# Kernel tuning notes

Measured on AMD Instinct MI355X. Metric: run time of the kernel, lower is better.

## Reference

```python
import jax, jax.numpy as jnp
import numpy as np

D_MODEL = 1024
N_HEADS = 16
D_K = D_MODEL // N_HEADS


def setup_inputs() -> dict:
    key = jax.random.key(0)
    k1, k2, k3, k4, k5 = jax.random.split(key, 5)
    B, S = 2, 2048
    scale = 1.0 / np.sqrt(D_MODEL)
    return {
        "query": jax.random.normal(k1, (B, S, D_MODEL), dtype=jnp.float32),
        "mask": jnp.ones((B, S, S), dtype=jnp.int32),
        "W_qkv": jax.random.normal(k2, (D_MODEL, 3 * D_MODEL), dtype=jnp.float32) * scale,
        "b_qkv": jax.random.normal(k3, (3 * D_MODEL,), dtype=jnp.float32) * 0.02,
        "W_out": jax.random.normal(k4, (D_MODEL, D_MODEL), dtype=jnp.float32) * scale,
        "b_out": jax.random.normal(k5, (D_MODEL,), dtype=jnp.float32) * 0.02,
    }


def reference(query, mask, W_qkv, b_qkv, W_out, b_out):
    B, S, _ = query.shape
    # fused QKV projection (all from query, matching the torch module)
    qkv = query @ W_qkv + b_qkv                      # [B, S, 3*D]
    q, k, v = jnp.split(qkv, 3, axis=-1)
    # [B, H, S, d_k]
    q = q.reshape(B, S, N_HEADS, D_K).transpose(0, 2, 1, 3)
    k = k.reshape(B, S, N_HEADS, D_K).transpose(0, 2, 1, 3)
    v = v.reshape(B, S, N_HEADS, D_K).transpose(0, 2, 1, 3)
    # scaled dot-product attention with explicit scores
    scores = jnp.einsum("bhqd,bhkd->bhqk", q, k) / jnp.sqrt(jnp.float32(D_K))
    m = mask[:, None, :, :]                           # [B, 1, S, S] broadcast over heads
    scores = jnp.where(m == 0, jnp.float32(-1e9), scores)
    attn = jax.nn.softmax(scores, axis=-1)           # dropout p=0 in eval -> identity
    ctx = jnp.einsum("bhqk,bhkd->bhqd", attn, v)     # [B, H, S, d_k]
    ctx = ctx.transpose(0, 2, 1, 3).reshape(B, S, D_MODEL)
    return ctx @ W_out + b_out
```

## Files before the change

kernel.cpp:

```cpp
#include <hip/hip_runtime.h>
#include <stdint.h>
#include <stddef.h>

#define S_LEN 2048
#define NB    2
#define DM    1024
#define NH    16
#define DKH   64
#define NTOK  4096
#define QKV_N 3072
#define QSCALE 0.18033688f

typedef __attribute__((ext_vector_type(4))) float floatx4;
using half2v = __attribute__((ext_vector_type(2))) _Float16;
using half4v = __attribute__((ext_vector_type(4))) _Float16;
using half8v = __attribute__((ext_vector_type(8))) _Float16;
using fp16x2 = __attribute__((ext_vector_type(2))) __fp16;

#if __has_builtin(__builtin_amdgcn_exp2f)
#define EXP2F __builtin_amdgcn_exp2f
#else
#define EXP2F exp2f
#endif

__device__ __forceinline__ void glds16(const void* g, void* l) {
    __builtin_amdgcn_global_load_lds((const __attribute__((address_space(1))) void*)g,
                                     (__attribute__((address_space(3))) void*)l,
                                     16, 0, 0);
}

__global__ __launch_bounds__(256) void cast_f16_kernel(const float* __restrict__ in,
                                                       _Float16* __restrict__ out, int n4) {
    int i = blockIdx.x * blockDim.x + threadIdx.x;
    if (i < n4) {
        float4 v = ((const float4*)in)[i];
        half4v o = {(_Float16)v.x, (_Float16)v.y, (_Float16)v.z, (_Float16)v.w};
        ((half4v*)out)[i] = o;
    }
}

__global__ __launch_bounds__(1024) void transpose_cast_kernel(const float* __restrict__ in,
                                                              _Float16* __restrict__ out,
                                                              int R, int C) {
    __shared__ float t[32][33];
    int c0 = blockIdx.x * 32, r0 = blockIdx.y * 32;
    int x = threadIdx.x, y = threadIdx.y;
    t[y][x] = in[(size_t)(r0 + y) * C + c0 + x];
    __syncthreads();
    out[(size_t)(c0 + y) * R + r0 + x] = (_Float16)t[x][y];
}

__global__ void flag_init_kernel(int* f) { *f = 1; }

__global__ __launch_bounds__(256) void mask_reduce_kernel(const int* __restrict__ mask,
                                                          int* __restrict__ f, int n4) {
    int i = blockIdx.x * blockDim.x + threadIdx.x;
    if (i < n4) {
        int4 v = ((const int4*)mask)[i];
        if (v.x == 0 || v.y == 0 || v.z == 0 || v.w == 0) *f = 0;
    }
}

template <int FINAL, int BN>
__global__ __launch_bounds__(256) void gemm_bt_kernel(const _Float16* __restrict__ A,
                                                      const _Float16* __restrict__ Bt,
                                                      const float* __restrict__ bias,
                                                      float* __restrict__ Cf,
                                                      _Float16* __restrict__ Ch,
                                                      _Float16* __restrict__ Vt,
                                                      int M, int N, int K) {
    constexpr int NJ = BN / 32;
    __shared__ _Float16 As[128 * 64];
    __shared__ _Float16 Bs[BN * 64];

    const int nt = blockIdx.x, mt = blockIdx.y;
    const int tid = threadIdx.x, wave = tid >> 6, lane = tid & 63;
    const int quad = lane >> 4, l16 = lane & 15;
    const int wm = wave >> 1, wn = wave & 1;

    floatx4 acc[4][NJ];
    #pragma unroll
    for (int i = 0; i < 4; ++i)
        #pragma unroll
        for (int j = 0; j < NJ; ++j)
            #pragma unroll
            for (int r = 0; r < 4; ++r) acc[i][j][r] = 0.0f;

    const _Float16* Ab = A + (size_t)mt * 128 * K;
    const _Float16* Bb = Bt + (size_t)nt * BN * K;

    for (int kt = 0; kt < K; kt += 64) {
        #pragma unroll
        for (int p = 0; p < 4; ++p) {
            int slot = p * 256 + wave * 64 + lane;
            int row = slot >> 3, cc = slot & 7, c = cc ^ (row & 7);
            glds16(Ab + (size_t)row * K + kt + c * 8, As + (size_t)(p * 256 + wave * 64) * 8);
        }
        #pragma unroll
        for (int p = 0; p < BN / 32; ++p) {
            int slot = p * 256 + wave * 64 + lane;
            int row = slot >> 3, cc = slot & 7, c = cc ^ (row & 7);
            glds16(Bb + (size_t)row * K + kt + c * 8, Bs + (size_t)(p * 256 + wave * 64) * 8);
        }
        __syncthreads();

        #pragma unroll
        for (int kk = 0; kk < 2; ++kk) {
            half8v af[4], bfr[NJ];
            #pragma unroll
            for (int i = 0; i < 4; ++i) {
                int row = wm * 64 + i * 16 + l16;
                int c = (kk * 4 + quad) ^ (row & 7);
                af[i] = *(const half8v*)(As + row * 64 + c * 8);
            }
            #pragma unroll
            for (int j = 0; j < NJ; ++j) {
                int row = wn * (BN / 2) + j * 16 + l16;
                int c = (kk * 4 + quad) ^ (row & 7);
                bfr[j] = *(const half8v*)(Bs + row * 64 + c * 8);
            }
            #pragma unroll
            for (int i = 0; i < 4; ++i)
                #pragma unroll
                for (int j = 0; j < NJ; ++j)
                    acc[i][j] = __builtin_amdgcn_mfma_f32_16x16x32_f16(af[i], bfr[j], acc[i][j], 0, 0, 0);
        }
        __syncthreads();
    }

    #pragma unroll
    for (int j = 0; j < NJ; ++j) {
        int n = nt * BN + wn * (BN / 2) + j * 16 + l16;
        float bv = bias[n];
        #pragma unroll
        for (int i = 0; i < 4; ++i) {
            int m0 = mt * 128 + wm * 64 + i * 16 + quad * 4;
            float v[4];
            #pragma unroll
            for (int r = 0; r < 4; ++r) v[r] = acc[i][j][r] + bv;
            if (FINAL) {
                #pragma unroll
                for (int r = 0; r < 4; ++r) Cf[(size_t)(m0 + r) * N + n] = v[r];
            } else {
                if (n < DM) {
                    #pragma unroll
                    for (int r = 0; r < 4; ++r) v[r] *= QSCALE;
                }
                if (n < 2 * DM) {
                    #pragma unroll
                    for (int r = 0; r < 4; ++r)
                        Ch[(size_t)(m0 + r) * QKV_N + n] = (_Float16)v[r];
                } else {
                    int bb = m0 >> 11, s = m0 & (S_LEN - 1);
                    half4v t = {(_Float16)v[0], (_Float16)v[1], (_Float16)v[2], (_Float16)v[3]};
                    *(half4v*)(Vt + ((size_t)bb * (NH * DKH) + (n - 2 * DM)) * S_LEN + s) = t;
                }
            }
        }
    }
}

__global__ __launch_bounds__(256) void flash_kernel(const _Float16* __restrict__ qkv,
                                                    const _Float16* __restrict__ vt,
                                                    const int* __restrict__ mask,
                                                    const int* __restrict__ flag,
                                                    _Float16* __restrict__ ctx) {
    __shared__ _Float16 Ks[128 * 64];
    __shared__ _Float16 Vs[64 * 128];

    const int qt = blockIdx.x, h = blockIdx.y, b = blockIdx.z;
    const int tid = threadIdx.x, wave = tid >> 6, lane = tid & 63;
    const int quad = lane >> 4, l16 = lane & 15;
    const int allones = *flag;

    const _Float16* qrow = qkv + (size_t)(b * S_LEN + qt * 64 + wave * 16 + l16) * QKV_N + h * DKH;
    half8v qf0 = *(const half8v*)(qrow + quad * 8);
    half8v qf1 = *(const half8v*)(qrow + 32 + quad * 8);

    floatx4 o[4];
    #pragma unroll
    for (int c = 0; c < 4; ++c)
        #pragma unroll
        for (int r = 0; r < 4; ++r) o[c][r] = 0.0f;
    float lsum = 0.0f;

    for (int kt = 0; kt < S_LEN / 128; ++kt) {
        #pragma unroll
        for (int p = 0; p < 4; ++p) {
            int slot = p * 256 + wave * 64 + lane;
            int row = slot >> 3, cc = slot & 7, c = cc ^ (row & 7);
            glds16(qkv + (size_t)(b * S_LEN + kt * 128 + row) * QKV_N + DM + h * DKH + c * 8,
                   Ks + (size_t)(p * 256 + wave * 64) * 8);
        }
        #pragma unroll
        for (int p = 0; p < 4; ++p) {
            int slot = p * 256 + wave * 64 + lane;
            int row = slot >> 4, cc = slot & 15, c = cc ^ (row & 15);
            glds16(vt + ((size_t)(b * NH + h) * DKH + row) * S_LEN + kt * 128 + c * 8,
                   Vs + (size_t)(p * 256 + wave * 64) * 8);
        }
        __syncthreads();

        floatx4 st[8];
        #pragma unroll
        for (int j = 0; j < 8; ++j) {
            int rowk = j * 16 + l16;
            half8v a0 = *(const half8v*)(Ks + rowk * 64 + ((quad) ^ (rowk & 7)) * 8);
            half8v a1 = *(const half8v*)(Ks + rowk * 64 + ((4 + quad) ^ (rowk & 7)) * 8);
            floatx4 z;
            #pragma unroll
            for (int r = 0; r < 4; ++r) z[r] = 0.0f;
            z = __builtin_amdgcn_mfma_f32_16x16x32_f16(a0, qf0, z, 0, 0, 0);
            z = __builtin_amdgcn_mfma_f32_16x16x32_f16(a1, qf1, z, 0, 0, 0);
            st[j] = z;
        }

        if (!allones) {
            for (int j = 0; j < 8; ++j)
                for (int r = 0; r < 4; ++r) {
                    int s = kt * 128 + j * 16 + quad * 4 + r;
                    int q = qt * 64 + wave * 16 + l16;
                    if (mask[((size_t)b * S_LEN + q) * S_LEN + s] == 0) st[j][r] = -1e9f;
                }
        }

        half4v pf[8];
        #pragma unroll
        for (int j = 0; j < 8; ++j) {
            float p0 = EXP2F(st[j][0]), p1 = EXP2F(st[j][1]);
            float p2 = EXP2F(st[j][2]), p3 = EXP2F(st[j][3]);
            lsum += (p0 + p1) + (p2 + p3);
            fp16x2 lo_n = __builtin_amdgcn_cvt_pkrtz(p0, p1);
            fp16x2 hi_n = __builtin_amdgcn_cvt_pkrtz(p2, p3);
            half2v lo = __builtin_bit_cast(half2v, lo_n);
            half2v hi = __builtin_bit_cast(half2v, hi_n);
            half4v pk = {lo.x, lo.y, hi.x, hi.y};
            pf[j] = pk;
        }

        #pragma unroll
        for (int j = 0; j < 8; ++j) {
            int g = 2 * j + (quad >> 1);
            #pragma unroll
            for (int c = 0; c < 4; ++c) {
                int rowv = c * 16 + l16;
                half4v bv = *(const half4v*)(Vs + rowv * 128 + ((g ^ (rowv & 15)) * 8) + (quad & 1) * 4);
                o[c] = __builtin_amdgcn_mfma_f32_16x16x16f16(pf[j], bv, o[c], 0, 0, 0);
            }
        }
        __syncthreads();
    }

    lsum += __shfl_xor(lsum, 16);
    lsum += __shfl_xor(lsum, 32);
    float linv[4];
    #pragma unroll
    for (int r = 0; r < 4; ++r)
        linv[r] = 1.0f / __shfl(lsum, (lane & 48) | ((lane >> 4) * 4 + r));

    #pragma unroll
    for (int c = 0; c < 4; ++c)
        #pragma unroll
        for (int r = 0; r < 4; ++r) {
            int q = qt * 64 + wave * 16 + quad * 4 + r;
            ctx[(size_t)(b * S_LEN + q) * DM + h * DKH + c * 16 + l16] =
                (_Float16)(o[c][r] * linv[r]);
        }
}

extern "C" void kernel_launch(void* const* d_in, const int* in_sizes, int n_in,
                              void* d_out, int out_size, void* d_ws, size_t ws_size,
                              hipStream_t stream) {
    const float* query = (const float*)d_in[0];
    const int*   mask  = (const int*)d_in[1];
    const float* W_qkv = (const float*)d_in[2];
    const float* b_qkv = (const float*)d_in[3];
    const float* W_out = (const float*)d_in[4];
    const float* b_out = (const float*)d_in[5];
    float* out = (float*)d_out;

    char* w = (char*)d_ws;
    _Float16* qh   = (_Float16*)w;  w += (size_t)NTOK * DM * 2;
    _Float16* wqt  = (_Float16*)w;  w += (size_t)QKV_N * DM * 2;
    _Float16* wot  = (_Float16*)w;  w += (size_t)DM * DM * 2;
    _Float16* qkvh = (_Float16*)w;  w += (size_t)NTOK * QKV_N * 2;
    _Float16* vt   = (_Float16*)w;  w += (size_t)NB * NH * DKH * S_LEN * 2;
    int*      flag = (int*)w;
    _Float16* ctxh = qh;

    cast_f16_kernel<<<(NTOK * DM / 4 + 255) / 256, 256, 0, stream>>>(query, qh, NTOK * DM / 4);
    transpose_cast_kernel<<<dim3(QKV_N / 32, DM / 32), dim3(32, 32), 0, stream>>>(W_qkv, wqt, DM, QKV_N);
    transpose_cast_kernel<<<dim3(DM / 32, DM / 32), dim3(32, 32), 0, stream>>>(W_out, wot, DM, DM);
    flag_init_kernel<<<1, 1, 0, stream>>>(flag);
    mask_reduce_kernel<<<(NB * S_LEN * S_LEN / 4 + 255) / 256, 256, 0, stream>>>(
        mask, flag, NB * S_LEN * S_LEN / 4);

    gemm_bt_kernel<0, 128><<<dim3(QKV_N / 128, NTOK / 128), 256, 0, stream>>>(
        qh, wqt, b_qkv, nullptr, qkvh, vt, NTOK, QKV_N, DM);

    flash_kernel<<<dim3(S_LEN / 64, NH, NB), 256, 0, stream>>>(qkvh, vt, mask, flag, ctxh);

    gemm_bt_kernel<1, 64><<<dim3(DM / 64, NTOK / 128), 256, 0, stream>>>(
        ctxh, wot, b_out, out, nullptr, nullptr, NTOK, DM, DM);
}
```

Baseline: 229.5 us.

## Process two query tiles per wave in flash attention to reuse K/V tiles

Each wave now handles 32 query rows instead of 16, so each block covers 128 queries and the grid halves. Every K and V fragment read from LDS feeds two MFMA streams, which halves the global-to-LDS K/V traffic per query. The cost is roughly double the accumulator and P registers per wave, which may lower occupancy, and fewer blocks (512) to spread across the CUs. The flag-init kernel is also replaced by hipMemsetAsync writing 0x01010101, and the flag check becomes a nonzero test to match.

```diff
diff --git a/kernel.cpp b/kernel.cpp
--- a/kernel.cpp
+++ b/kernel.cpp
@@ -49,8 +49,6 @@
     __syncthreads();
     out[(size_t)(c0 + y) * R + r0 + x] = (_Float16)t[x][y];
 }
-
-__global__ void flag_init_kernel(int* f) { *f = 1; }
 
 __global__ __launch_bounds__(256) void mask_reduce_kernel(const int* __restrict__ mask,
                                                           int* __restrict__ f, int n4) {
@@ -171,18 +169,21 @@
     const int qt = blockIdx.x, h = blockIdx.y, b = blockIdx.z;
     const int tid = threadIdx.x, wave = tid >> 6, lane = tid & 63;
     const int quad = lane >> 4, l16 = lane & 15;
-    const int allones = *flag;
-
-    const _Float16* qrow = qkv + (size_t)(b * S_LEN + qt * 64 + wave * 16 + l16) * QKV_N + h * DKH;
-    half8v qf0 = *(const half8v*)(qrow + quad * 8);
-    half8v qf1 = *(const half8v*)(qrow + 32 + quad * 8);
-
-    floatx4 o[4];
+    const int allones = (*flag != 0);
+
+    const _Float16* qrow0 = qkv + (size_t)(b * S_LEN + qt * 128 + wave * 32 + l16) * QKV_N + h * DKH;
+    const _Float16* qrow1 = qrow0 + (size_t)16 * QKV_N;
+    half8v qa0 = *(const half8v*)(qrow0 + quad * 8);
+    half8v qa1 = *(const half8v*)(qrow0 + 32 + quad * 8);
+    half8v qb0 = *(const half8v*)(qrow1 + quad * 8);
+    half8v qb1 = *(const half8v*)(qrow1 + 32 + quad * 8);
+
+    floatx4 oa[4], ob[4];
     #pragma unroll
     for (int c = 0; c < 4; ++c)
         #pragma unroll
-        for (int r = 0; r < 4; ++r) o[c][r] = 0.0f;
-    float lsum = 0.0f;
+        for (int r = 0; r < 4; ++r) { oa[c][r] = 0.0f; ob[c][r] = 0.0f; }
+    float lsa = 0.0f, lsb = 0.0f;
 
     for (int kt = 0; kt < S_LEN / 128; ++kt) {
         #pragma unroll
@@ -201,41 +202,46 @@
         }
         __syncthreads();
 
-        floatx4 st[8];
+        half4v pa[8], pb[8];
         #pragma unroll
         for (int j = 0; j < 8; ++j) {
             int rowk = j * 16 + l16;
             half8v a0 = *(const half8v*)(Ks + rowk * 64 + ((quad) ^ (rowk & 7)) * 8);
             half8v a1 = *(const half8v*)(Ks + rowk * 64 + ((4 + quad) ^ (rowk & 7)) * 8);
-            floatx4 z;
-            #pragma unroll
-            for (int r = 0; r < 4; ++r) z[r] = 0.0f;
-            z = __builtin_amdgcn_mfma_f32_16x16x32_f16(a0, qf0, z, 0, 0, 0);
-            z = __builtin_amdgcn_mfma_f32_16x16x32_f16(a1, qf1, z, 0, 0, 0);
-            st[j] = z;
-        }
-
-        if (!allones) {
-            for (int j = 0; j < 8; ++j)
+            floatx4 za, zb;
+            #pragma unroll
+            for (int r = 0; r < 4; ++r) { za[r] = 0.0f; zb[r] = 0.0f; }
+            za = __builtin_amdgcn_mfma_f32_16x16x32_f16(a0, qa0, za, 0, 0, 0);
+            za = __builtin_amdgcn_mfma_f32_16x16x32_f16(a1, qa1, za, 0, 0, 0);
+            zb = __builtin_amdgcn_mfma_f32_16x16x32_f16(a0, qb0, zb, 0, 0, 0);
+            zb = __builtin_amdgcn_mfma_f32_16x16x32_f16(a1, qb1, zb, 0, 0, 0);
+
+            if (!allones) {
                 for (int r = 0; r < 4; ++r) {
                     int s = kt * 128 + j * 16 + quad * 4 + r;
-                    int q = qt * 64 + wave * 16 + l16;
-                    if (mask[((size_t)b * S_LEN + q) * S_LEN + s] == 0) st[j][r] = -1e9f;
+                    int qA = qt * 128 + wave * 32 + l16;
+                    if (mask[((size_t)b * S_LEN + qA) * S_LEN + s] == 0) za[r] = -1e9f;
+                    if (mask[((size_t)b * S_LEN + qA + 16) * S_LEN + s] == 0) zb[r] = -1e9f;
                 }
-        }
-
-        half4v pf[8];
-        #pragma unroll
-        for (int j = 0; j < 8; ++j) {
-            float p0 = EXP2F(st[j][0]), p1 = EXP2F(st[j][1]);
-            float p2 = EXP2F(st[j][2]), p3 = EXP2F(st[j][3]);
-            lsum += (p0 + p1) + (p2 + p3);
-            fp16x2 lo_n = __builtin_amdgcn_cvt_pkrtz(p0, p1);
-            fp16x2 hi_n = __builtin_amdgcn_cvt_pkrtz(p2, p3);
-            half2v lo = __builtin_bit_cast(half2v, lo_n);
-            half2v hi = __builtin_bit_cast(half2v, hi_n);
-            half4v pk = {lo.x, lo.y, hi.x, hi.y};
-            pf[j] = pk;
+            }
+
+            float p0 = EXP2F(za[0]), p1 = EXP2F(za[1]), p2 = EXP2F(za[2]), p3 = EXP2F(za[3]);
+            lsa += (p0 + p1) + (p2 + p3);
+            fp16x2 lo = __builtin_amdgcn_cvt_pkrtz(p0, p1);
+            fp16x2 hi = __builtin_amdgcn_cvt_pkrtz(p2, p3);
+            half2v lo2 = __builtin_bit_cast(half2v, lo);
+            half2v hi2 = __builtin_bit_cast(half2v, hi);
+            half4v pka = {lo2.x, lo2.y, hi2.x, hi2.y};
+            pa[j] = pka;
+
+            p0 = EXP2F(zb[0]); p1 = EXP2F(zb[1]); p2 = EXP2F(zb[2]); p3 = EXP2F(zb[3]);
+            lsb += (p0 + p1) + (p2 + p3);
+            lo = __builtin_amdgcn_cvt_pkrtz(p0, p1);
+            hi = __builtin_amdgcn_cvt_pkrtz(p2, p3);
+            lo2 = __builtin_bit_cast(half2v, lo);
+            hi2 = __builtin_bit_cast(half2v, hi);
+            half4v pkb = {lo2.x, lo2.y, hi2.x, hi2.y};
+            pb[j] = pkb;
         }
 
         #pragma unroll
@@ -245,26 +251,31 @@
             for (int c = 0; c < 4; ++c) {
                 int rowv = c * 16 + l16;
                 half4v bv = *(const half4v*)(Vs + rowv * 128 + ((g ^ (rowv & 15)) * 8) + (quad & 1) * 4);
-                o[c] = __builtin_amdgcn_mfma_f32_16x16x16f16(pf[j], bv, o[c], 0, 0, 0);
+                oa[c] = __builtin_amdgcn_mfma_f32_16x16x16f16(pa[j], bv, oa[c], 0, 0, 0);
+                ob[c] = __builtin_amdgcn_mfma_f32_16x16x16f16(pb[j], bv, ob[c], 0, 0, 0);
             }
         }
         __syncthreads();
     }
 
-    lsum += __shfl_xor(lsum, 16);
-    lsum += __shfl_xor(lsum, 32);
-    float linv[4];
-    #pragma unroll
-    for (int r = 0; r < 4; ++r)
-        linv[r] = 1.0f / __shfl(lsum, (lane & 48) | ((lane >> 4) * 4 + r));
+    lsa += __shfl_xor(lsa, 16); lsa += __shfl_xor(lsa, 32);
+    lsb += __shfl_xor(lsb, 16); lsb += __shfl_xor(lsb, 32);
+    float lia[4], lib[4];
+    #pragma unroll
+    for (int r = 0; r < 4; ++r) {
+        int src = (lane & 48) | ((lane >> 4) * 4 + r);
+        lia[r] = 1.0f / __shfl(lsa, src);
+        lib[r] = 1.0f / __shfl(lsb, src);
+    }
 
     #pragma unroll
     for (int c = 0; c < 4; ++c)
         #pragma unroll
         for (int r = 0; r < 4; ++r) {
-            int q = qt * 64 + wave * 16 + quad * 4 + r;
-            ctx[(size_t)(b * S_LEN + q) * DM + h * DKH + c * 16 + l16] =
-                (_Float16)(o[c][r] * linv[r]);
+            int qA = qt * 128 + wave * 32 + quad * 4 + r;
+            int col = h * DKH + c * 16 + l16;
+            ctx[(size_t)(b * S_LEN + qA) * DM + col]        = (_Float16)(oa[c][r] * lia[r]);
+            ctx[(size_t)(b * S_LEN + qA + 16) * DM + col]   = (_Float16)(ob[c][r] * lib[r]);
         }
 }
 
@@ -291,14 +302,14 @@
     cast_f16_kernel<<<(NTOK * DM / 4 + 255) / 256, 256, 0, stream>>>(query, qh, NTOK * DM / 4);
     transpose_cast_kernel<<<dim3(QKV_N / 32, DM / 32), dim3(32, 32), 0, stream>>>(W_qkv, wqt, DM, QKV_N);
     transpose_cast_kernel<<<dim3(DM / 32, DM / 32), dim3(32, 32), 0, stream>>>(W_out, wot, DM, DM);
-    flag_init_kernel<<<1, 1, 0, stream>>>(flag);
+    hipMemsetAsync(flag, 1, 4, stream);
     mask_reduce_kernel<<<(NB * S_LEN * S_LEN / 4 + 255) / 256, 256, 0, stream>>>(
         mask, flag, NB * S_LEN * S_LEN / 4);
 
     gemm_bt_kernel<0, 128><<<dim3(QKV_N / 128, NTOK / 128), 256, 0, stream>>>(
         qh, wqt, b_qkv, nullptr, qkvh, vt, NTOK, QKV_N, DM);
 
-    flash_kernel<<<dim3(S_LEN / 64, NH, NB), 256, 0, stream>>>(qkvh, vt, mask, flag, ctxh);
+    flash_kernel<<<dim3(S_LEN / 128, NH, NB), 256, 0, stream>>>(qkvh, vt, mask, flag, ctxh);
 
     gemm_bt_kernel<1, 64><<<dim3(DM / 64, NTOK / 128), 256, 0, stream>>>(
         ctxh, wot, b_out, out, nullptr, nullptr, NTOK, DM, DM);
```

Result: faster. 219.0 us (-4.6%).

## Give each flash wave 64 query rows to reuse K/V tile fragments

Applied to the files above, without the earlier changes.

The flash attention kernel moves from 4 waves of 16 query rows each to 2 waves (128 threads) that each handle 64 query rows as four 16-row groups. Each K fragment and V fragment read from LDS then feeds four MFMAs, which cuts LDS traffic per FLOP and doubles the query tile per block to 128 rows. The grid is reordered so blocks of the same batch and head are adjacent, and the flag init kernel becomes a hipMemsetAsync with byte value 1, which is nonzero and so still reads as all-ones. In exchange, register pressure rises sharply (16 accumulator vectors plus 8 Q fragments per lane), and there are half as many blocks.

```diff
diff --git a/kernel.cpp b/kernel.cpp
--- a/kernel.cpp
+++ b/kernel.cpp
@@ -49,8 +49,6 @@
     __syncthreads();
     out[(size_t)(c0 + y) * R + r0 + x] = (_Float16)t[x][y];
 }
-
-__global__ void flag_init_kernel(int* f) { *f = 1; }
 
 __global__ __launch_bounds__(256) void mask_reduce_kernel(const int* __restrict__ mask,
                                                           int* __restrict__ f, int n4) {
@@ -160,7 +158,7 @@
     }
 }
 
-__global__ __launch_bounds__(256) void flash_kernel(const _Float16* __restrict__ qkv,
+__global__ __launch_bounds__(128) void flash_kernel(const _Float16* __restrict__ qkv,
                                                     const _Float16* __restrict__ vt,
                                                     const int* __restrict__ mask,
                                                     const int* __restrict__ flag,
@@ -168,104 +166,111 @@
     __shared__ _Float16 Ks[128 * 64];
     __shared__ _Float16 Vs[64 * 128];
 
-    const int qt = blockIdx.x, h = blockIdx.y, b = blockIdx.z;
+    const int bh = blockIdx.x, qt = blockIdx.y;
+    const int b = bh >> 4, h = bh & 15;
     const int tid = threadIdx.x, wave = tid >> 6, lane = tid & 63;
     const int quad = lane >> 4, l16 = lane & 15;
-    const int allones = *flag;
-
-    const _Float16* qrow = qkv + (size_t)(b * S_LEN + qt * 64 + wave * 16 + l16) * QKV_N + h * DKH;
-    half8v qf0 = *(const half8v*)(qrow + quad * 8);
-    half8v qf1 = *(const half8v*)(qrow + 32 + quad * 8);
-
-    floatx4 o[4];
-    #pragma unroll
-    for (int c = 0; c < 4; ++c)
-        #pragma unroll
-        for (int r = 0; r < 4; ++r) o[c][r] = 0.0f;
-    float lsum = 0.0f;
+    const int allones = (*flag != 0);
+
+    half8v qf0[4], qf1[4];
+    #pragma unroll
+    for (int G = 0; G < 4; ++G) {
+        const _Float16* qr = qkv + (size_t)(b * S_LEN + qt * 128 + wave * 64 + G * 16 + l16) * QKV_N + h * DKH;
+        qf0[G] = *(const half8v*)(qr + quad * 8);
+        qf1[G] = *(const half8v*)(qr + 32 + quad * 8);
+    }
+
+    const _Float16* kbase = qkv + (size_t)b * S_LEN * QKV_N + DM + h * DKH;
+    const _Float16* vbase = vt + (size_t)(b * NH + h) * DKH * S_LEN;
+
+    floatx4 o[4][4];
+    #pragma unroll
+    for (int G = 0; G < 4; ++G)
+        #pragma unroll
+        for (int c = 0; c < 4; ++c)
+            #pragma unroll
+            for (int r = 0; r < 4; ++r) o[G][c][r] = 0.0f;
+    float ls[4] = {0.0f, 0.0f, 0.0f, 0.0f};
 
     for (int kt = 0; kt < S_LEN / 128; ++kt) {
         #pragma unroll
-        for (int p = 0; p < 4; ++p) {
-            int slot = p * 256 + wave * 64 + lane;
+        for (int p = 0; p < 8; ++p) {
+            int slot = p * 128 + tid;
             int row = slot >> 3, cc = slot & 7, c = cc ^ (row & 7);
-            glds16(qkv + (size_t)(b * S_LEN + kt * 128 + row) * QKV_N + DM + h * DKH + c * 8,
-                   Ks + (size_t)(p * 256 + wave * 64) * 8);
-        }
-        #pragma unroll
-        for (int p = 0; p < 4; ++p) {
-            int slot = p * 256 + wave * 64 + lane;
+            glds16(kbase + (size_t)(kt * 128 + row) * QKV_N + c * 8, Ks + (size_t)slot * 8);
+        }
+        #pragma unroll
+        for (int p = 0; p < 8; ++p) {
+            int slot = p * 128 + tid;
             int row = slot >> 4, cc = slot & 15, c = cc ^ (row & 15);
-            glds16(vt + ((size_t)(b * NH + h) * DKH + row) * S_LEN + kt * 128 + c * 8,
-                   Vs + (size_t)(p * 256 + wave * 64) * 8);
+            glds16(vbase + (size_t)row * S_LEN + kt * 128 + c * 8, Vs + (size_t)slot * 8);
         }
         __syncthreads();
 
-        floatx4 st[8];
         #pragma unroll
         for (int j = 0; j < 8; ++j) {
             int rowk = j * 16 + l16;
             half8v a0 = *(const half8v*)(Ks + rowk * 64 + ((quad) ^ (rowk & 7)) * 8);
             half8v a1 = *(const half8v*)(Ks + rowk * 64 + ((4 + quad) ^ (rowk & 7)) * 8);
-            floatx4 z;
-            #pragma unroll
-            for (int r = 0; r < 4; ++r) z[r] = 0.0f;
-            z = __builtin_amdgcn_mfma_f32_16x16x32_f16(a0, qf0, z, 0, 0, 0);
-            z = __builtin_amdgcn_mfma_f32_16x16x32_f16(a1, qf1, z, 0, 0, 0);
-            st[j] = z;
-        }
-
-        if (!allones) {
-            for (int j = 0; j < 8; ++j)
-                for (int r = 0; r < 4; ++r) {
-                    int s = kt * 128 + j * 16 + quad * 4 + r;
-                    int q = qt * 64 + wave * 16 + l16;
-                    if (mask[((size_t)b * S_LEN + q) * S_LEN + s] == 0) st[j][r] = -1e9f;
+
+            half4v pk[4];
+            #pragma unroll
+            for (int G = 0; G < 4; ++G) {
+                floatx4 z;
+                #pragma unroll
+                for (int r = 0; r < 4; ++r) z[r] = 0.0f;
+                z = __builtin_amdgcn_mfma_f32_16x16x32_f16(a0, qf0[G], z, 0, 0, 0);
+                z = __builtin_amdgcn_mfma_f32_16x16x32_f16(a1, qf1[G], z, 0, 0, 0);
+
+                if (!allones) {
+                    for (int r = 0; r < 4; ++r) {
+                        int s = kt * 128 + j * 16 + quad * 4 + r;
+                        int qA = qt * 128 + wave * 64 + G * 16 + l16;
+                        if (mask[((size_t)b * S_LEN + qA) * S_LEN + s] == 0) z[r] = -1e9f;
+                    }
                 }
-        }
-
-        half4v pf[8];
-        #pragma unroll
-        for (int j = 0; j < 8; ++j) {
-            float p0 = EXP2F(st[j][0]), p1 = EXP2F(st[j][1]);
-            float p2 = EXP2F(st[j][2]), p3 = EXP2F(st[j][3]);
-            lsum += (p0 + p1) + (p2 + p3);
-            fp16x2 lo_n = __builtin_amdgcn_cvt_pkrtz(p0, p1);
-            fp16x2 hi_n = __builtin_amdgcn_cvt_pkrtz(p2, p3);
-            half2v lo = __builtin_bit_cast(half2v, lo_n);
-            half2v hi = __builtin_bit_cast(half2v, hi_n);
-            half4v pk = {lo.x, lo.y, hi.x, hi.y};
-            pf[j] = pk;
-        }
-
-        #pragma unroll
-        for (int j = 0; j < 8; ++j) {
+
+                float p0 = EXP2F(z[0]), p1 = EXP2F(z[1]), p2 = EXP2F(z[2]), p3 = EXP2F(z[3]);
+                ls[G] += (p0 + p1) + (p2 + p3);
+                fp16x2 lo = __builtin_amdgcn_cvt_pkrtz(p0, p1);
+                fp16x2 hi = __builtin_amdgcn_cvt_pkrtz(p2, p3);
+                half2v lo2 = __builtin_bit_cast(half2v, lo);
+                half2v hi2 = __builtin_bit_cast(half2v, hi);
+                half4v pkg = {lo2.x, lo2.y, hi2.x, hi2.y};
+                pk[G] = pkg;
+            }
+
             int g = 2 * j + (quad >> 1);
             #pragma unroll
             for (int c = 0; c < 4; ++c) {
                 int rowv = c * 16 + l16;
                 half4v bv = *(const half4v*)(Vs + rowv * 128 + ((g ^ (rowv & 15)) * 8) + (quad & 1) * 4);
-                o[c] = __builtin_amdgcn_mfma_f32_16x16x16f16(pf[j], bv, o[c], 0, 0, 0);
+                #pragma unroll
+                for (int G = 0; G < 4; ++G)
+                    o[G][c] = __builtin_amdgcn_mfma_f32_16x16x16f16(pk[G], bv, o[G][c], 0, 0, 0);
             }
         }
         __syncthreads();
     }
 
-    lsum += __shfl_xor(lsum, 16);
-    lsum += __shfl_xor(lsum, 32);
-    float linv[4];
-    #pragma unroll
-    for (int r = 0; r < 4; ++r)
-        linv[r] = 1.0f / __shfl(lsum, (lane & 48) | ((lane >> 4) * 4 + r));
-
-    #pragma unroll
-    for (int c = 0; c < 4; ++c)
-        #pragma unroll
-        for (int r = 0; r < 4; ++r) {
-            int q = qt * 64 + wave * 16 + quad * 4 + r;
-            ctx[(size_t)(b * S_LEN + q) * DM + h * DKH + c * 16 + l16] =
-                (_Float16)(o[c][r] * linv[r]);
-        }
+    #pragma unroll
+    for (int G = 0; G < 4; ++G) {
+        float l = ls[G];
+        l += __shfl_xor(l, 16);
+        l += __shfl_xor(l, 32);
+        float linv[4];
+        #pragma unroll
+        for (int r = 0; r < 4; ++r)
+            linv[r] = 1.0f / __shfl(l, (lane & 48) | ((lane >> 4) * 4 + r));
+        #pragma unroll
+        for (int c = 0; c < 4; ++c)
+            #pragma unroll
+            for (int r = 0; r < 4; ++r) {
+                int qA = qt * 128 + wave * 64 + G * 16 + quad * 4 + r;
+                ctx[(size_t)(b * S_LEN + qA) * DM + h * DKH + c * 16 + l16] =
+                    (_Float16)(o[G][c][r] * linv[r]);
+            }
+    }
 }
 
 extern "C" void kernel_launch(void* const* d_in, const int* in_sizes, int n_in,
@@ -291,14 +296,14 @@
     cast_f16_kernel<<<(NTOK * DM / 4 + 255) / 256, 256, 0, stream>>>(query, qh, NTOK * DM / 4);
     transpose_cast_kernel<<<dim3(QKV_N / 32, DM / 32), dim3(32, 32), 0, stream>>>(W_qkv, wqt, DM, QKV_N);
     transpose_cast_kernel<<<dim3(DM / 32, DM / 32), dim3(32, 32), 0, stream>>>(W_out, wot, DM, DM);
-    flag_init_kernel<<<1, 1, 0, stream>>>(flag);
+    hipMemsetAsync(flag, 1, 4, stream);
     mask_reduce_kernel<<<(NB * S_LEN * S_LEN / 4 + 255) / 256, 256, 0, stream>>>(
         mask, flag, NB * S_LEN * S_LEN / 4);
 
     gemm_bt_kernel<0, 128><<<dim3(QKV_N / 128, NTOK / 128), 256, 0, stream>>>(
         qh, wqt, b_qkv, nullptr, qkvh, vt, NTOK, QKV_N, DM);
 
-    flash_kernel<<<dim3(S_LEN / 64, NH, NB), 256, 0, stream>>>(qkvh, vt, mask, flag, ctxh);
+    flash_kernel<<<dim3(NB * NH, S_LEN / 128), 128, 0, stream>>>(qkvh, vt, mask, flag, ctxh);
 
     gemm_bt_kernel<1, 64><<<dim3(DM / 64, NTOK / 128), 256, 0, stream>>>(
         ctxh, wot, b_out, out, nullptr, nullptr, NTOK, DM, DM);
```

Measured after the change: 232.1 us. About the same (+1.1%).
